# Optimization experiments

Hardware: AMD Instinct MI355X
Metric: run time of the kernel (lower is better)

## Reference

```python
import jax, jax.numpy as jnp
import numpy as np

HEAD, SIZE = 16, 64
DIM = HEAD * SIZE
NINF = -10000.0
EPS = 1e-6


def setup_inputs() -> dict:
    key = jax.random.key(0)
    ks = jax.random.split(key, 12)
    B, S = 4, 2048
    std = 0.02
    return {
        "x": jax.random.normal(ks[0], (B, S, DIM), jnp.float32),
        "mask": jax.random.randint(ks[1], (B, S), 0, 2, jnp.int32),
        "wq_w": jax.random.normal(ks[2], (DIM, DIM), jnp.float32) * std,
        "wq_b": jnp.zeros((DIM,), jnp.float32),
        "wk_w": jax.random.normal(ks[3], (DIM, DIM), jnp.float32) * std,
        "wk_b": jnp.zeros((DIM,), jnp.float32),
        "wv_w": jax.random.normal(ks[4], (DIM, DIM), jnp.float32) * std,
        "wv_b": jnp.zeros((DIM,), jnp.float32),
        "dense_w": jax.random.normal(ks[5], (DIM, DIM), jnp.float32) * std,
        "dense_b": jnp.zeros((DIM,), jnp.float32),
        "gamma": jnp.ones((DIM,), jnp.float32),
        "beta": jnp.zeros((DIM,), jnp.float32),
    }


def _split_heads(t):
    # [B, S, DIM] -> [B, H, S, size]
    B, S, _ = t.shape
    return t.reshape(B, S, HEAD, SIZE).transpose(0, 2, 1, 3)


def _layernorm(x, gamma, beta):
    mu = jnp.mean(x, axis=-1, keepdims=True)
    var = jnp.mean(jnp.square(x - mu), axis=-1, keepdims=True)
    return (x - mu) * jax.lax.rsqrt(var + EPS) * gamma + beta


def reference(x, mask, wq_w, wq_b, wk_w, wk_b, wv_w, wv_b, dense_w, dense_b, gamma, beta):
    B, S, _ = x.shape
    q = _split_heads(x @ wq_w + wq_b)
    k = _split_heads(x @ wk_w + wk_b)
    v = _split_heads(x @ wv_w + wv_b)
    # scores [B, H, S, S]
    scores = jnp.einsum("bhqd,bhkd->bhqk", q, k) / jnp.sqrt(jnp.float32(SIZE))
    scores = scores + mask.astype(jnp.float32)[:, None, None, :] * NINF
    attn = jax.nn.softmax(scores, axis=-1)
    ctx = jnp.einsum("bhqk,bhkd->bhqd", attn, v)  # [B, H, S, size]
    ctx = ctx.transpose(0, 2, 1, 3).reshape(B, S, DIM)
    out = _layernorm(x + (ctx @ dense_w + dense_b), gamma, beta)
    return out, attn
```

## Files before the change

kernel.cpp:

```cpp
#include <hip/hip_runtime.h>
#include <stdint.h>

#define NB 4
#define NS 2048
#define NH 16
#define HSZ 64
#define ND 1024
#define NM (NB*NS)
#define QSCALE 0.180336880f
#define MADD2 -14426.950409f

typedef unsigned short u16;
typedef unsigned int u32;
typedef __attribute__((ext_vector_type(4))) float f32x4;
typedef __attribute__((ext_vector_type(8))) __bf16 bf16x8;

static __device__ __forceinline__ u16 f2bf(float f){
  unsigned int x = __builtin_bit_cast(unsigned int, f);
  x += 0x7fffu + ((x >> 16) & 1u);
  return (u16)(x >> 16);
}
static __device__ __forceinline__ u16 f2bf_rz(float f){
  return (u16)(__builtin_bit_cast(unsigned int, f) >> 16);
}

#define GLDS16(gp, lp) __builtin_amdgcn_global_load_lds( \
    (const __attribute__((address_space(1))) void*)(gp),  \
    (__attribute__((address_space(3))) void*)(lp), 16, 0, 0)

__global__ __launch_bounds__(256) void k_cast(const float4* __restrict__ in,
                                              ushort4* __restrict__ out, int n4){
  int i = blockIdx.x*256 + threadIdx.x;
  if (i >= n4) return;
  float4 v = in[i];
  ushort4 o;
  o.x = f2bf(v.x); o.y = f2bf(v.y); o.z = f2bf(v.z); o.w = f2bf(v.w);
  out[i] = o;
}

__global__ __launch_bounds__(256) void k_transpose4(const float* __restrict__ wq,
    const float* __restrict__ wk, const float* __restrict__ wv,
    const float* __restrict__ wd, u16* __restrict__ wcat, u16* __restrict__ wdt){
  __shared__ float t[32][33];
  const int z = blockIdx.z;
  const float* in = (z==0) ? wq : (z==1) ? wk : (z==2) ? wv : wd;
  u16* out = (z<3) ? (wcat + (size_t)z*ND*ND) : wdt;
  int tx = threadIdx.x & 31, ty = threadIdx.x >> 5;
  int n0 = blockIdx.x*32, k0 = blockIdx.y*32;
  #pragma unroll
  for (int i=0;i<32;i+=8)
    t[ty+i][tx] = in[(size_t)(k0+ty+i)*ND + n0 + tx];
  __syncthreads();
  #pragma unroll
  for (int i=0;i<32;i+=8)
    out[(size_t)(n0+ty+i)*ND + k0 + tx] = f2bf(t[tx][ty+i]);
}

template<int EPI>
__global__ __launch_bounds__(256,2) void k_gemm(const u16* __restrict__ A,
    const u16* __restrict__ Bt, const float* __restrict__ b0,
    const float* __restrict__ b1, const float* __restrict__ b2,
    const float* __restrict__ resid, u16* __restrict__ Qo, u16* __restrict__ Ko,
    u16* __restrict__ Vto, float* __restrict__ Out){
  __shared__ u16 sAB[2][128*64];
  u16* sA = sAB[0];
  u16* sB = sAB[1];
  const int tid = threadIdx.x;
  const int wave = tid >> 6, lane = tid & 63;
  const int l15 = lane & 15, l4 = lane >> 4;
  const int m0 = blockIdx.x * 128, n0 = blockIdx.y * 128;
  const int wm = wave >> 1, wn = wave & 1;
  const f32x4 vz = {0.f,0.f,0.f,0.f};
  f32x4 acc[4][4];
  #pragma unroll
  for (int i=0;i<4;i++)
    #pragma unroll
    for (int j=0;j<4;j++) acc[i][j] = vz;

  for (int k0 = 0; k0 < 1024; k0 += 64){
    __syncthreads();
    #pragma unroll
    for (int t=0; t<4; t++){
      const int jb = (t*4 + wave)*64;
      const int j  = jb + lane;
      const int r = j >> 3, c = (j & 7) << 3;
      GLDS16(A  + (((size_t)(m0 + r)) << 10) + (size_t)(k0 + c), sA + jb*8);
      GLDS16(Bt + (((size_t)(n0 + r)) << 10) + (size_t)(k0 + c), sB + jb*8);
    }
    __syncthreads();
    #pragma unroll
    for (int kk=0; kk<64; kk+=32){
      bf16x8 af[4], bv[4];
      #pragma unroll
      for (int mi=0;mi<4;mi++)
        af[mi] = *(const bf16x8*)(const void*)(sA + (wm*64 + mi*16 + l15)*64 + kk + l4*8);
      #pragma unroll
      for (int ni=0;ni<4;ni++)
        bv[ni] = *(const bf16x8*)(const void*)(sB + (wn*64 + ni*16 + l15)*64 + kk + l4*8);
      #pragma unroll
      for (int mi=0;mi<4;mi++)
        #pragma unroll
        for (int ni=0;ni<4;ni++)
          acc[mi][ni] = __builtin_amdgcn_mfma_f32_16x16x32_bf16(af[mi], bv[ni], acc[mi][ni], 0, 0, 0);
    }
  }

  if (EPI == 0){
    const int sec = n0 >> 10;
    const float* bias = (sec==0) ? b0 : (sec==1) ? b1 : b2;
    const float scale = (sec==0) ? QSCALE : 1.0f;
    if (sec < 2){
      u16* dst = (sec==0) ? Qo : Ko;
      #pragma unroll
      for (int mi=0;mi<4;mi++){
        #pragma unroll
        for (int ni=0;ni<4;ni++){
          const int n = n0 + wn*64 + ni*16 + l15;
          const int nn = n & (ND-1);
          const int h = nn >> 6, d = nn & 63;
          const float bvv = bias[nn];
          #pragma unroll
          for (int j=0;j<4;j++){
            const int m = m0 + wm*64 + mi*16 + l4*4 + j;
            const int b = m >> 11, s = m & (NS-1);
            const float v = (acc[mi][ni][j] + bvv) * scale;
            dst[((((size_t)b*NH + h)*NS + s) << 6) + d] = f2bf(v);
          }
        }
      }
    } else {
      __syncthreads();
      u16 (*sT)[128] = (u16(*)[128])sAB;
      #pragma unroll
      for (int mi=0;mi<4;mi++){
        #pragma unroll
        for (int ni=0;ni<4;ni++){
          const int nl = wn*64 + ni*16 + l15;
          const float bvv = bias[(n0 & (ND-1)) + nl];
          #pragma unroll
          for (int j=0;j<4;j++){
            const int ml = wm*64 + mi*16 + l4*4 + j;
            sT[nl][ml] = f2bf(acc[mi][ni][j] + bvv);
          }
        }
      }
      __syncthreads();
      const int nbase = n0 & (ND-1);
      const int b2 = m0 >> 11;
      const int sbase = m0 & (NS-1);
      #pragma unroll
      for (int it=0; it<8; ++it){
        const int idx = it*256 + tid;
        const int row = idx >> 4;
        const int ch  = (idx & 15) << 3;
        const int nn2 = nbase + row;
        const int h2 = nn2 >> 6, d2 = nn2 & 63;
        *(int4*)(void*)(Vto + ((((size_t)b2*NH + h2)*HSZ + d2) << 11) + sbase + ch)
            = *(const int4*)(const void*)&sT[row][ch];
      }
    }
  } else {
    #pragma unroll
    for (int mi=0;mi<4;mi++){
      #pragma unroll
      for (int ni=0;ni<4;ni++){
        const int n = n0 + wn*64 + ni*16 + l15;
        const float bvv = b0[n];
        #pragma unroll
        for (int j=0;j<4;j++){
          const int m = m0 + wm*64 + mi*16 + l4*4 + j;
          const size_t o = ((size_t)m << 10) + n;
          Out[o] = acc[mi][ni][j] + bvv + resid[o];
        }
      }
    }
  }
}

static __device__ __forceinline__ void attn_decode(int bid, int& qb, int& bh){
  const int x = bid & 7, t = bid >> 3;
  qb = t & 15;
  bh = (t >> 4) * 8 + x;
}

__global__ __launch_bounds__(512,4) void k_attn_fused(const u16* __restrict__ Q,
    const u16* __restrict__ K, const u16* __restrict__ Vt,
    const int* __restrict__ mask, float* __restrict__ attn, u16* __restrict__ ctx){
  __shared__ u16 sK[2][64][72];
  __shared__ u16 sV[2][64][72];
  __shared__ u16 sP[8][16][72];
  __shared__ float sMadd[NS];
  const int tid = threadIdx.x, wave = tid>>6, lane = tid&63;
  const int l15 = lane&15, l4 = lane>>4;
  int qb, bh; attn_decode(blockIdx.x, qb, bh);
  const int b = bh >> 4, h = bh & 15;
  const size_t hoff = (size_t)bh * NS * HSZ;
  const int q0 = qb*128 + wave*16;
  const u16* Kg = K + hoff;
  const u16* Vg = Vt + hoff;
  const bf16x8 qf0 = *(const bf16x8*)(const void*)(Q + hoff + (size_t)(q0+l15)*HSZ + l4*8);
  const bf16x8 qf1 = *(const bf16x8*)(const void*)(Q + hoff + (size_t)(q0+l15)*HSZ + 32 + l4*8);
  const f32x4 vz = {0.f,0.f,0.f,0.f};
  const int r = tid >> 3, c = (tid & 7) << 3;

  #pragma unroll
  for (int t=0;t<4;t++){
    const int kk = t*512 + tid;
    sMadd[kk] = mask[b*NS + kk] ? MADD2 : 0.f;
  }

  float lr[4] = {0.f,0.f,0.f,0.f};
  {
    int4 rK = *(const int4*)(const void*)(Kg + (size_t)r*HSZ + c);
    *(int4*)(void*)&sK[0][r][c] = rK;
    rK = *(const int4*)(const void*)(Kg + (size_t)(64+r)*HSZ + c);
    __syncthreads();
    for (int kb=0; kb<NS; kb+=64){
      const int cur = (kb>>6)&1;
      if (kb+64 < NS)
        *(int4*)(void*)&sK[cur^1][r][c] = rK;
      if (kb+128 < NS)
        rK = *(const int4*)(const void*)(Kg + (size_t)(kb+128+r)*HSZ + c);
      #pragma unroll
      for (int n=0;n<4;n++){
        bf16x8 kf0 = *(const bf16x8*)(const void*)&sK[cur][n*16+l15][l4*8];
        bf16x8 kf1 = *(const bf16x8*)(const void*)&sK[cur][n*16+l15][32+l4*8];
        f32x4 a = vz;
        a = __builtin_amdgcn_mfma_f32_16x16x32_bf16(qf0, kf0, a, 0,0,0);
        a = __builtin_amdgcn_mfma_f32_16x16x32_bf16(qf1, kf1, a, 0,0,0);
        const float madd = sMadd[kb + n*16 + l15];
        #pragma unroll
        for (int j=0;j<4;j++)
          lr[j] += __builtin_amdgcn_exp2f(a[j] + madd);
      }
      __syncthreads();
    }
  }
  float rinv[4];
  #pragma unroll
  for (int j=0;j<4;j++){
    float l = lr[j];
    #pragma unroll
    for (int off=1; off<16; off<<=1)
      l += __shfl_xor(l, off, 64);
    rinv[j] = 1.f/l;
  }

  f32x4 cacc[4];
  #pragma unroll
  for (int i=0;i<4;i++) cacc[i] = vz;
  float* attn_base = attn + (size_t)bh * NS * NS;

  int4 rK = *(const int4*)(const void*)(Kg + (size_t)r*HSZ + c);
  int4 rV = *(const int4*)(const void*)(Vg + (size_t)r*NS + c);
  *(int4*)(void*)&sK[0][r][c] = rK;
  *(int4*)(void*)&sV[0][r][c] = rV;
  rK = *(const int4*)(const void*)(Kg + (size_t)(64+r)*HSZ + c);
  rV = *(const int4*)(const void*)(Vg + (size_t)r*NS + 64 + c);
  __syncthreads();

  for (int kb=0; kb<NS; kb+=64){
    const int cur = (kb>>6)&1;
    if (kb+64 < NS){
      *(int4*)(void*)&sK[cur^1][r][c] = rK;
      *(int4*)(void*)&sV[cur^1][r][c] = rV;
    }
    if (kb+128 < NS){
      rK = *(const int4*)(const void*)(Kg + (size_t)(kb+128+r)*HSZ + c);
      rV = *(const int4*)(const void*)(Vg + (size_t)r*NS + (kb+128) + c);
    }
    #pragma unroll
    for (int n=0;n<4;n++){
      bf16x8 kf0 = *(const bf16x8*)(const void*)&sK[cur][n*16+l15][l4*8];
      bf16x8 kf1 = *(const bf16x8*)(const void*)&sK[cur][n*16+l15][32+l4*8];
      f32x4 a = vz;
      a = __builtin_amdgcn_mfma_f32_16x16x32_bf16(qf0, kf0, a, 0,0,0);
      a = __builtin_amdgcn_mfma_f32_16x16x32_bf16(qf1, kf1, a, 0,0,0);
      const float madd = sMadd[kb + n*16 + l15];
      #pragma unroll
      for (int j=0;j<4;j++){
        const float e = __builtin_amdgcn_exp2f(a[j] + madd);
        sP[wave][l4*4+j][n*16+l15] = f2bf_rz(e * rinv[j]);
      }
    }
    #pragma unroll
    for (int kk=0;kk<2;kk++){
      bf16x8 pf = *(const bf16x8*)(const void*)&sP[wave][l15][kk*32 + l4*8];
      #pragma unroll
      for (int n2=0;n2<4;n2++){
        bf16x8 vf = *(const bf16x8*)(const void*)&sV[cur][n2*16+l15][kk*32 + l4*8];
        cacc[n2] = __builtin_amdgcn_mfma_f32_16x16x32_bf16(pf, vf, cacc[n2], 0,0,0);
      }
    }
    #pragma unroll
    for (int jj=0;jj<4;jj++){
      const int rr = jj*4 + l4;
      const uint2 pw = *(const uint2*)(const void*)&sP[wave][rr][l15*4];
      f32x4 o;
      o.x = __builtin_bit_cast(float, pw.x << 16);
      o.y = __builtin_bit_cast(float, pw.x & 0xffff0000u);
      o.z = __builtin_bit_cast(float, pw.y << 16);
      o.w = __builtin_bit_cast(float, pw.y & 0xffff0000u);
      __builtin_nontemporal_store(o,
          (f32x4*)(void*)&attn_base[(size_t)(q0 + rr)*NS + kb + l15*4]);
    }
    __syncthreads();
  }
  #pragma unroll
  for (int n2=0;n2<4;n2++)
    #pragma unroll
    for (int j=0;j<4;j++){
      const int q = q0 + l4*4 + j;
      ctx[(((size_t)(b*NS + q)) << 10) + h*HSZ + n2*16 + l15] = f2bf(cacc[n2][j]);
    }
}

__global__ __launch_bounds__(256) void k_layernorm(float* __restrict__ buf,
    const float* __restrict__ gamma, const float* __restrict__ beta){
  const int row = blockIdx.x, tid = threadIdx.x;
  float4* rp = (float4*)(buf + ((size_t)row << 10));
  float4 a = rp[tid];
  float s  = a.x + a.y + a.z + a.w;
  float ss = a.x*a.x + a.y*a.y + a.z*a.z + a.w*a.w;
  #pragma unroll
  for (int off=1; off<64; off<<=1){
    s  += __shfl_xor(s,  off, 64);
    ss += __shfl_xor(ss, off, 64);
  }
  __shared__ float red[8];
  const int wave = tid>>6, lane = tid&63;
  if (lane == 0){ red[wave] = s; red[wave+4] = ss; }
  __syncthreads();
  s  = red[0]+red[1]+red[2]+red[3];
  ss = red[4]+red[5]+red[6]+red[7];
  const float mu  = s * (1.f/1024.f);
  const float var = ss * (1.f/1024.f) - mu*mu;
  const float rs  = rsqrtf(var + 1e-6f);
  float4 g  = ((const float4*)gamma)[tid];
  float4 be = ((const float4*)beta)[tid];
  f32x4 o;
  o.x = (a.x-mu)*rs*g.x + be.x;
  o.y = (a.y-mu)*rs*g.y + be.y;
  o.z = (a.z-mu)*rs*g.z + be.z;
  o.w = (a.w-mu)*rs*g.w + be.w;
  __builtin_nontemporal_store(o, (f32x4*)(void*)&rp[tid]);
}

extern "C" void kernel_launch(void* const* d_in, const int* in_sizes, int n_in,
                              void* d_out, int out_size, void* d_ws, size_t ws_size,
                              hipStream_t stream){
  const float* x     = (const float*)d_in[0];
  const int*   mask  = (const int*)d_in[1];
  const float* wq_w  = (const float*)d_in[2];
  const float* wq_b  = (const float*)d_in[3];
  const float* wk_w  = (const float*)d_in[4];
  const float* wk_b  = (const float*)d_in[5];
  const float* wv_w  = (const float*)d_in[6];
  const float* wv_b  = (const float*)d_in[7];
  const float* wd_w  = (const float*)d_in[8];
  const float* wd_b  = (const float*)d_in[9];
  const float* gamma = (const float*)d_in[10];
  const float* beta  = (const float*)d_in[11];

  float* out0 = (float*)d_out;
  float* attn = out0 + (size_t)NM * ND;

  char* ws = (char*)d_ws;
  u16*   xb    = (u16*)(ws);
  u16*   ctx   = (u16*)(ws);
  u16*   wcat  = (u16*)(ws + (16u<<20));
  u16*   wdt   = (u16*)(ws + (22u<<20));
  u16*   Qb    = (u16*)(ws + (24u<<20));
  u16*   Kb    = (u16*)(ws + (40u<<20));
  u16*   Vtb   = (u16*)(ws + (56u<<20));

  k_cast<<<8192, 256, 0, stream>>>((const float4*)x, (ushort4*)xb, NM*ND/4);
  k_transpose4<<<dim3(32,32,4), 256, 0, stream>>>(wq_w, wk_w, wv_w, wd_w, wcat, wdt);

  k_gemm<0><<<dim3(64,24), 256, 0, stream>>>(xb, wcat, wq_b, wk_b, wv_b,
                                             nullptr, Qb, Kb, Vtb, nullptr);

  k_attn_fused<<<1024, 512, 0, stream>>>(Qb, Kb, Vtb, mask, attn, ctx);

  k_gemm<2><<<dim3(64,8), 256, 0, stream>>>(ctx, wdt, wd_b, nullptr, nullptr,
                                            x, nullptr, nullptr, nullptr, out0);
  k_layernorm<<<NM, 256, 0, stream>>>(out0, gamma, beta);
}
```

Before: 365.9 us.

## Merge prep kernels, remap QKV GEMM tiles per XCD, stage Q/K stores via LDS

The x cast and the weight transposes now run in a single launch, with a fifth z-slice doing a grid-stride bf16 cast, which saves one kernel launch. The QKV GEMM uses a 1D grid whose blocks are remapped so that each XCD handles a contiguous group of tiles, aimed at better L2 reuse of A and B. The Q/K epilogue now stages the tile through shared memory and writes 16-byte vectorized rows instead of scattered 2-byte stores. The cost is an extra LDS pass and barrier in the epilogue and a less parallel cast slice.

After: 369.3 us. Within noise of the previous version (+0.9%).

```diff
diff --git a/kernel.cpp b/kernel.cpp
--- a/kernel.cpp
+++ b/kernel.cpp
@@ -28,21 +28,24 @@
     (const __attribute__((address_space(1))) void*)(gp),  \
     (__attribute__((address_space(3))) void*)(lp), 16, 0, 0)
 
-__global__ __launch_bounds__(256) void k_cast(const float4* __restrict__ in,
-                                              ushort4* __restrict__ out, int n4){
-  int i = blockIdx.x*256 + threadIdx.x;
-  if (i >= n4) return;
-  float4 v = in[i];
-  ushort4 o;
-  o.x = f2bf(v.x); o.y = f2bf(v.y); o.z = f2bf(v.z); o.w = f2bf(v.w);
-  out[i] = o;
-}
-
-__global__ __launch_bounds__(256) void k_transpose4(const float* __restrict__ wq,
-    const float* __restrict__ wk, const float* __restrict__ wv,
-    const float* __restrict__ wd, u16* __restrict__ wcat, u16* __restrict__ wdt){
+__global__ __launch_bounds__(256) void k_prep(const float* __restrict__ x,
+    const float* __restrict__ wq, const float* __restrict__ wk,
+    const float* __restrict__ wv, const float* __restrict__ wd,
+    u16* __restrict__ xb, u16* __restrict__ wcat, u16* __restrict__ wdt){
   __shared__ float t[32][33];
   const int z = blockIdx.z;
+  if (z == 4){
+    const float4* in4 = (const float4*)x;
+    ushort4* out4 = (ushort4*)xb;
+    const int n4 = NM*ND/4;
+    for (int i = (blockIdx.y*32 + blockIdx.x)*256 + threadIdx.x; i < n4; i += 1024*256){
+      float4 v = in4[i];
+      ushort4 o;
+      o.x = f2bf(v.x); o.y = f2bf(v.y); o.z = f2bf(v.z); o.w = f2bf(v.w);
+      out4[i] = o;
+    }
+    return;
+  }
   const float* in = (z==0) ? wq : (z==1) ? wk : (z==2) ? wv : wd;
   u16* out = (z<3) ? (wcat + (size_t)z*ND*ND) : wdt;
   int tx = threadIdx.x & 31, ty = threadIdx.x >> 5;
@@ -68,7 +71,17 @@
   const int tid = threadIdx.x;
   const int wave = tid >> 6, lane = tid & 63;
   const int l15 = lane & 15, l4 = lane >> 4;
-  const int m0 = blockIdx.x * 128, n0 = blockIdx.y * 128;
+  int bx, by;
+  if (EPI == 0){
+    const int xcd = blockIdx.x & 7, t = blockIdx.x >> 3;
+    const int st = t / 48, loc = t % 48;
+    const int gs = xcd*4 + st;
+    bx = (gs & 7)*8 + (loc & 7);
+    by = (gs >> 3)*6 + (loc >> 3);
+  } else {
+    bx = blockIdx.x; by = blockIdx.y;
+  }
+  const int m0 = bx * 128, n0 = by * 128;
   const int wm = wave >> 1, wn = wave & 1;
   const f32x4 vz = {0.f,0.f,0.f,0.f};
   f32x4 acc[4][4];
@@ -109,34 +122,45 @@
     const int sec = n0 >> 10;
     const float* bias = (sec==0) ? b0 : (sec==1) ? b1 : b2;
     const float scale = (sec==0) ? QSCALE : 1.0f;
+    const int nbase = n0 & (ND-1);
+    const int b2 = m0 >> 11;
+    const int sbase = m0 & (NS-1);
+    __syncthreads();
     if (sec < 2){
       u16* dst = (sec==0) ? Qo : Ko;
-      #pragma unroll
-      for (int mi=0;mi<4;mi++){
-        #pragma unroll
-        for (int ni=0;ni<4;ni++){
-          const int n = n0 + wn*64 + ni*16 + l15;
-          const int nn = n & (ND-1);
-          const int h = nn >> 6, d = nn & 63;
-          const float bvv = bias[nn];
-          #pragma unroll
-          for (int j=0;j<4;j++){
-            const int m = m0 + wm*64 + mi*16 + l4*4 + j;
-            const int b = m >> 11, s = m & (NS-1);
-            const float v = (acc[mi][ni][j] + bvv) * scale;
-            dst[((((size_t)b*NH + h)*NS + s) << 6) + d] = f2bf(v);
-          }
-        }
-      }
-    } else {
-      __syncthreads();
       u16 (*sT)[128] = (u16(*)[128])sAB;
       #pragma unroll
       for (int mi=0;mi<4;mi++){
         #pragma unroll
         for (int ni=0;ni<4;ni++){
           const int nl = wn*64 + ni*16 + l15;
-          const float bvv = bias[(n0 & (ND-1)) + nl];
+          const float bvv = bias[nbase + nl];
+          #pragma unroll
+          for (int j=0;j<4;j++){
+            const int ml = wm*64 + mi*16 + l4*4 + j;
+            sT[ml][nl] = f2bf((acc[mi][ni][j] + bvv) * scale);
+          }
+        }
+      }
+      __syncthreads();
+      const int h0 = nbase >> 6;
+      #pragma unroll
+      for (int it=0; it<8; ++it){
+        const int idx = it*256 + tid;
+        const int row = idx >> 4;
+        const int h2  = (idx >> 3) & 1;
+        const int d8  = (idx & 7) << 3;
+        *(int4*)(void*)(dst + ((((size_t)b2*NH + h0+h2)*NS + sbase+row) << 6) + d8)
+            = *(const int4*)(const void*)&sT[row][h2*64 + d8];
+      }
+    } else {
+      u16 (*sT)[128] = (u16(*)[128])sAB;
+      #pragma unroll
+      for (int mi=0;mi<4;mi++){
+        #pragma unroll
+        for (int ni=0;ni<4;ni++){
+          const int nl = wn*64 + ni*16 + l15;
+          const float bvv = bias[nbase + nl];
           #pragma unroll
           for (int j=0;j<4;j++){
             const int ml = wm*64 + mi*16 + l4*4 + j;
@@ -145,9 +169,6 @@
         }
       }
       __syncthreads();
-      const int nbase = n0 & (ND-1);
-      const int b2 = m0 >> 11;
-      const int sbase = m0 & (NS-1);
       #pragma unroll
       for (int it=0; it<8; ++it){
         const int idx = it*256 + tid;
@@ -374,11 +395,11 @@
   u16*   Kb    = (u16*)(ws + (40u<<20));
   u16*   Vtb   = (u16*)(ws + (56u<<20));
 
-  k_cast<<<8192, 256, 0, stream>>>((const float4*)x, (ushort4*)xb, NM*ND/4);
-  k_transpose4<<<dim3(32,32,4), 256, 0, stream>>>(wq_w, wk_w, wv_w, wd_w, wcat, wdt);
-
-  k_gemm<0><<<dim3(64,24), 256, 0, stream>>>(xb, wcat, wq_b, wk_b, wv_b,
-                                             nullptr, Qb, Kb, Vtb, nullptr);
+  k_prep<<<dim3(32,32,5), 256, 0, stream>>>(x, wq_w, wk_w, wv_w, wd_w,
+                                            xb, wcat, wdt);
+
+  k_gemm<0><<<1536, 256, 0, stream>>>(xb, wcat, wq_b, wk_b, wv_b,
+                                      nullptr, Qb, Kb, Vtb, nullptr);
 
   k_attn_fused<<<1024, 512, 0, stream>>>(Qb, Kb, Vtb, mask, attn, ctx);
 
```
